# Performance work log

Hardware: AMD Instinct MI355X
Metric: run time of the kernel (lower is better)

The kernel has to match this reference:

```python
import jax, jax.numpy as jnp
import numpy as np

B, N, CIN, D, K, H, W = 1, 65536, 5, 128, 16, 64, 1024
EPS = 1e-5


def _bn(x, g, b, m, v, ch_axis):
    shape = [1] * x.ndim
    shape[ch_axis] = -1
    return (x - m.reshape(shape)) * jax.lax.rsqrt(v.reshape(shape) + EPS) * g.reshape(shape) + b.reshape(shape)


def setup_inputs() -> dict:
    key = jax.random.key(0)
    ks = jax.random.split(key, 10)
    s = 0.05
    return {
        "pc": jax.random.normal(ks[0], (B, N, CIN), jnp.float32),
        "neighbors": jax.random.randint(ks[1], (B, N, K), 0, N),
        "px": jax.random.randint(ks[2], (N,), 0, W),
        "py": jax.random.randint(ks[3], (N,), 0, H),
        "norm_gamma": jnp.ones((CIN,), jnp.float32),
        "norm_beta": jnp.zeros((CIN,), jnp.float32),
        "norm_mean": jnp.zeros((CIN,), jnp.float32),
        "norm_var": jnp.ones((CIN,), jnp.float32),
        "conv1_w": jax.random.normal(ks[4], (D, CIN), jnp.float32) * s,
        "conv1_b": jnp.zeros((D,), jnp.float32),
        "bn2a_gamma": jnp.ones((CIN,), jnp.float32),
        "bn2a_beta": jnp.zeros((CIN,), jnp.float32),
        "bn2a_mean": jnp.zeros((CIN,), jnp.float32),
        "bn2a_var": jnp.ones((CIN,), jnp.float32),
        "w2a": jax.random.normal(ks[5], (D, CIN), jnp.float32) * s,
        "bn2b_gamma": jnp.ones((D,), jnp.float32),
        "bn2b_beta": jnp.zeros((D,), jnp.float32),
        "bn2b_mean": jnp.zeros((D,), jnp.float32),
        "bn2b_var": jnp.ones((D,), jnp.float32),
        "w2b": jax.random.normal(ks[6], (D, D), jnp.float32) * s,
        "final_w": jax.random.normal(ks[7], (D, 2 * D), jnp.float32) * s,
        "final_b": jnp.zeros((D,), jnp.float32),
    }


def reference(pc, neighbors, px, py,
              norm_gamma, norm_beta, norm_mean, norm_var,
              conv1_w, conv1_b,
              bn2a_gamma, bn2a_beta, bn2a_mean, bn2a_var, w2a,
              bn2b_gamma, bn2b_beta, bn2b_mean, bn2b_var, w2b,
              final_w, final_b):
    # pc: [B, N, CIN] -> channels-first [B, CIN, N]
    x = jnp.transpose(pc, (0, 2, 1))
    x = _bn(x, norm_gamma, norm_beta, norm_mean, norm_var, 1)  # BatchNorm1d (eval)
    # point embedding: 1x1 conv1d
    point_emb = jnp.einsum('dc,bcn->bdn', conv1_w, x) + conv1_b[None, :, None]
    # neighbor gather (skip self at k=0): idx [B, K-1, N]
    nb = jnp.transpose(neighbors, (0, 2, 1))
    idx = nb[:, 1:, :]
    # gathered: [B, CIN, K-1, N]
    gathered = jnp.take_along_axis(x[:, :, None, :], idx[:, None, :, :], axis=3)
    neigh = gathered - x[:, :, None, :]  # per-neighbor difference
    # shared MLP: BN2d -> 1x1 conv (no bias) -> BN2d -> GELU -> 1x1 conv (no bias)
    h = _bn(neigh, bn2a_gamma, bn2a_beta, bn2a_mean, bn2a_var, 1)
    h = jnp.einsum('dc,bckn->bdkn', w2a, h)
    h = _bn(h, bn2b_gamma, bn2b_beta, bn2b_mean, bn2b_var, 1)
    h = jax.nn.gelu(h, approximate=False)  # torch nn.GELU default = exact erf
    h = jnp.einsum('ed,bdkn->bekn', w2b, h)
    neigh_emb = jnp.max(h, axis=2)  # max over neighbors -> [B, D, N]
    feats = jnp.einsum('df,bfn->bdn', final_w,
                       jnp.concatenate([point_emb, neigh_emb], axis=1)) + final_b[None, :, None]
    # scatter into range image (B assumed 1, as in original squeeze(0))
    proj = jnp.full((H, W, D), -1.0, dtype=jnp.float32)
    proj = proj.at[py, px].set(feats[0].T)
    return jnp.transpose(proj, (2, 0, 1))[None]  # [1, D, H, W]
```

## Files before the change

kernel.cpp:

```cpp
#include <hip/hip_runtime.h>

#define NPTS 65536
#define WW 1024
#define HWCELLS 65536
#define EPSF 1e-5f
#define QPTS 16

typedef __attribute__((ext_vector_type(8))) short short8;
typedef __attribute__((ext_vector_type(4))) float f32x4;

__device__ __forceinline__ float gelu_f(float x) {
    float x2 = x * x;
    float q  = fmaf(x2, -0.1029432f, -2.3022160f);
    float e  = __builtin_amdgcn_exp2f(x * q);
    float r  = __builtin_amdgcn_rcpf(1.0f + e);
    return x * r;
}
__device__ __forceinline__ unsigned f2bf_rne(float x) {
    unsigned u = __float_as_uint(x);
    return (u + 0x7fffu + ((u >> 16) & 1u)) >> 16;
}
__device__ __forceinline__ unsigned cvtpk(float lo, float hi) {
    unsigned r;
    asm("v_cvt_pk_bf16_f32 %0, %1, %2" : "=v"(r) : "v"(lo), "v"(hi));
    return r;
}

__global__ void init_out_k(float4* __restrict__ out4, int* __restrict__ winner) {
    int i = blockIdx.x * 256 + threadIdx.x;
    out4[i] = make_float4(-1.f, -1.f, -1.f, -1.f);
    if (i < HWCELLS) winner[i] = -1;
}

__global__ void prep_k(const float* __restrict__ pc, const int* __restrict__ px,
                       const int* __restrict__ py,
                       float4* __restrict__ xn4, float* __restrict__ xn1,
                       int* __restrict__ winner) {
    int i = blockIdx.x * blockDim.x + threadIdx.x;
    if (i >= NPTS) return;
    const float* p = &pc[(size_t)i * 5];
    xn4[i] = make_float4(p[0], p[1], p[2], p[3]);
    xn1[i] = p[4];
    int cell = py[i] * WW + px[i];
    atomicMax(&winner[cell], i);
}

__global__ void cnt_k(const int* __restrict__ winner, int* __restrict__ blockcnt) {
    int cell = blockIdx.x * 256 + threadIdx.x;
    bool occ = winner[cell] >= 0;
    unsigned long long m = __ballot(occ);
    __shared__ int wcnt[4];
    int lane = threadIdx.x & 63, wv = threadIdx.x >> 6;
    if (lane == 0) wcnt[wv] = __popcll(m);
    __syncthreads();
    if (threadIdx.x == 0)
        blockcnt[blockIdx.x] = wcnt[0] + wcnt[1] + wcnt[2] + wcnt[3];
}

__global__ void scan_k(const int* __restrict__ blockcnt, int* __restrict__ blockoff,
                       int* __restrict__ count) {
    __shared__ int s[256];
    int t = threadIdx.x;
    int orig = blockcnt[t];
    s[t] = orig;
    __syncthreads();
    for (int off = 1; off < 256; off <<= 1) {
        int v = (t >= off) ? s[t - off] : 0;
        __syncthreads();
        s[t] += v;
        __syncthreads();
    }
    blockoff[t] = s[t] - orig;
    if (t == 255) *count = s[255];
}

__global__ void fill_k(const int* __restrict__ winner, const int* __restrict__ blockoff,
                       int* __restrict__ ids) {
    int cell = blockIdx.x * 256 + threadIdx.x;
    int win = winner[cell];
    bool occ = win >= 0;
    unsigned long long m = __ballot(occ);
    __shared__ int wcnt[4];
    int lane = threadIdx.x & 63, wv = threadIdx.x >> 6;
    if (lane == 0) wcnt[wv] = __popcll(m);
    __syncthreads();
    int woff = blockoff[blockIdx.x];
    for (int i = 0; i < wv; ++i) woff += wcnt[i];
    if (occ) {
        int lrank = __popcll(m & ((1ull << lane) - 1));
        ids[woff + lrank] = win;
    }
}

__global__ void pad_k(int* __restrict__ ids, const int* __restrict__ count) {
    int c = *count;
    int i = c + threadIdx.x;
    if (threadIdx.x < 16 && i < NPTS) ids[i] = ids[0];
}

__global__ void fold_k(const float* __restrict__ ng, const float* __restrict__ nbta,
                       const float* __restrict__ nm, const float* __restrict__ nv,
                       const float* __restrict__ w2a,
                       const float* __restrict__ g2a, const float* __restrict__ b2a,
                       const float* __restrict__ m2a, const float* __restrict__ v2a,
                       const float* __restrict__ g2b, const float* __restrict__ b2b,
                       const float* __restrict__ m2b, const float* __restrict__ v2b,
                       const float* __restrict__ w2b,
                       const float* __restrict__ c1w, const float* __restrict__ c1b,
                       const float* __restrict__ fw, const float* __restrict__ fbias,
                       unsigned short* __restrict__ w2aB8,
                       unsigned short* __restrict__ w2bB,
                       unsigned short* __restrict__ fwallB) {
    __shared__ float c1wS[640];
    __shared__ float c1adjS[128];
    int d = threadIdx.x;

    float s_n[5], t_n[5];
#pragma unroll
    for (int c = 0; c < 5; ++c) {
        s_n[c] = ng[c] * rsqrtf(nv[c] + EPSF);
        t_n[c] = nbta[c] - nm[c] * s_n[c];
    }
    for (int j = d; j < 640; j += 128) c1wS[j] = c1w[j];
    __syncthreads();
    {
        float a = c1b[d];
#pragma unroll
        for (int c = 0; c < 5; ++c) a += c1wS[d * 5 + c] * t_n[c];
        c1adjS[d] = a;
    }
    __syncthreads();

    float s2b = g2b[d] * rsqrtf(v2b[d] + EPSF);
    float t2b = b2b[d] - m2b[d] * s2b;
    float acc = 0.f;
#pragma unroll
    for (int c = 0; c < 5; ++c) {
        float s2a = g2a[c] * rsqrtf(v2a[c] + EPSF);
        float t2a = b2a[c] - m2a[c] * s2a;
        float wv = w2a[d * 5 + c];
        w2aB8[d * 8 + c] = (unsigned short)f2bf_rne(s2b * wv * s2a * s_n[c]);
        acc += s2b * wv * t2a;
    }
    w2aB8[d * 8 + 5] = (unsigned short)f2bf_rne(acc + t2b);
    w2aB8[d * 8 + 6] = 0; w2aB8[d * 8 + 7] = 0;

#pragma unroll 8
    for (int i4 = 0; i4 < 32; ++i4) {
        float4 v = *(const float4*)&w2b[d * 128 + i4 * 4];
        unsigned short* dst = &w2bB[d * 128 + i4 * 4];
        dst[0] = (unsigned short)f2bf_rne(v.x);
        dst[1] = (unsigned short)f2bf_rne(v.y);
        dst[2] = (unsigned short)f2bf_rne(v.z);
        dst[3] = (unsigned short)f2bf_rne(v.w);
    }

    float f1[5] = {0.f, 0.f, 0.f, 0.f, 0.f};
    float fbv = fbias[d];
#pragma unroll 8
    for (int d4 = 0; d4 < 32; ++d4) {
        float4 fv = *(const float4*)&fw[d * 256 + d4 * 4];
        float4 fn = *(const float4*)&fw[d * 256 + 128 + d4 * 4];
        unsigned short* dst = &fwallB[d * 160 + d4 * 4];
        dst[0] = (unsigned short)f2bf_rne(fn.x);
        dst[1] = (unsigned short)f2bf_rne(fn.y);
        dst[2] = (unsigned short)f2bf_rne(fn.z);
        dst[3] = (unsigned short)f2bf_rne(fn.w);
        int dd = d4 * 4;
        fbv += fv.x * c1adjS[dd] + fv.y * c1adjS[dd+1] + fv.z * c1adjS[dd+2] + fv.w * c1adjS[dd+3];
#pragma unroll
        for (int c = 0; c < 5; ++c)
            f1[c] += fv.x * c1wS[dd*5 + c] + fv.y * c1wS[(dd+1)*5 + c]
                   + fv.z * c1wS[(dd+2)*5 + c] + fv.w * c1wS[(dd+3)*5 + c];
    }
#pragma unroll
    for (int c = 0; c < 5; ++c)
        fwallB[d * 160 + 128 + c] = (unsigned short)f2bf_rne(f1[c] * s_n[c]);
    fwallB[d * 160 + 133] = (unsigned short)f2bf_rne(fbv);
    for (int j = 134; j < 160; ++j) fwallB[d * 160 + j] = 0;
}

__launch_bounds__(256, 6)
__global__ void main_k(const int* __restrict__ ids, const int* __restrict__ countp,
                       const int* __restrict__ nbrs,
                       const float4* __restrict__ xn4, const float* __restrict__ xn1,
                       const int* __restrict__ px, const int* __restrict__ py,
                       const unsigned short* __restrict__ w2aB8,
                       const unsigned short* __restrict__ w2bB,
                       const unsigned short* __restrict__ fwallB,
                       float* __restrict__ outp) {
    const int n0 = blockIdx.x * QPTS;
    if (n0 >= *countp) return;

    __shared__ char           lds[8192];
    __shared__ unsigned short dxS[15 * 16 * 8];
    __shared__ int   idS[QPTS];
    __shared__ int   nbS[QPTS * 16];
    __shared__ float xnS[QPTS][5];
    __shared__ int   cellS[QPTS];

    const int t = threadIdx.x;
    const int w = t >> 6;
    const int l = t & 63;
    const int l15 = l & 15;
    const int lg  = l >> 4;

    if (t < QPTS) idS[t] = ids[n0 + t];
    __syncthreads();

    nbS[t] = nbrs[idS[t >> 4] * 16 + (t & 15)];
    if (t < QPTS) {
        int id = idS[t];
        float4 a = xn4[id];
        xnS[t][0] = a.x; xnS[t][1] = a.y; xnS[t][2] = a.z; xnS[t][3] = a.w;
        xnS[t][4] = xn1[id];
        cellS[t] = py[id] * WW + px[id];
    }

    short8 a1[2] = { {0,0,0,0,0,0,0,0}, {0,0,0,0,0,0,0,0} };
    if (lg == 0) {
        a1[0] = *(const short8*)(w2aB8 + (w * 32 + l15) * 8);
        a1[1] = *(const short8*)(w2aB8 + (w * 32 + 16 + l15) * 8);
    }
    short8 a2[2][4];
#pragma unroll
    for (int rt = 0; rt < 2; ++rt)
#pragma unroll
        for (int ks = 0; ks < 4; ++ks)
            a2[rt][ks] = *(const short8*)(w2bB + (w * 32 + rt * 16 + l15) * 128 + ks * 32 + lg * 8);

    __syncthreads();

    if (t < 240) {
        int pt = t & 15, kk = t >> 4;
        int nb = nbS[pt * 16 + kk + 1];
        float4 a = xn4[nb];
        float  e = xn1[nb];
        float d0 = a.x - xnS[pt][0];
        float d1 = a.y - xnS[pt][1];
        float d2 = a.z - xnS[pt][2];
        float d3 = a.w - xnS[pt][3];
        float d4 = e   - xnS[pt][4];
        uint4 v;
        v.x = cvtpk(d0, d1);
        v.y = cvtpk(d2, d3);
        v.z = cvtpk(d4, 1.0f);
        v.w = 0u;
        *(uint4*)&dxS[(kk * 16 + pt) * 8] = v;
    }
    __syncthreads();

    const f32x4 zero4 = {0.f, 0.f, 0.f, 0.f};
    f32x4 mmax[2];
#pragma unroll
    for (int rt = 0; rt < 2; ++rt)
#pragma unroll
        for (int j = 0; j < 4; ++j) mmax[rt][j] = -1e30f;

    for (int kk = 0; kk < 15; ++kk) {
        short8 dxf = *(const short8*)&dxS[(kk * 16 + l15) * 8];
        char* Gb = lds + (kk & 1) * 4096;
#pragma unroll
        for (int rt = 0; rt < 2; ++rt) {
            f32x4 s = __builtin_amdgcn_mfma_f32_16x16x32_bf16(a1[rt], dxf, zero4, 0, 0, 0);
            uint2 pr;
            pr.x = cvtpk(gelu_f(s[0]), gelu_f(s[1]));
            pr.y = cvtpk(gelu_f(s[2]), gelu_f(s[3]));
            int din0 = w * 32 + rt * 16 + lg * 4;
            *(uint2*)(Gb + l15 * 256 + ((din0 * 2) ^ (l15 << 4))) = pr;
        }
        __syncthreads();
        f32x4 acc[2];
#pragma unroll
        for (int ks = 0; ks < 4; ++ks) {
            int kb = (ks * 32 + lg * 8) * 2;
            short8 bfrag = *(const short8*)(Gb + l15 * 256 + (kb ^ (l15 << 4)));
#pragma unroll
            for (int rt = 0; rt < 2; ++rt)
                acc[rt] = __builtin_amdgcn_mfma_f32_16x16x32_bf16(
                    a2[rt][ks], bfrag, ks == 0 ? zero4 : acc[rt], 0, 0, 0);
        }
#pragma unroll
        for (int rt = 0; rt < 2; ++rt)
#pragma unroll
            for (int j = 0; j < 4; ++j)
                mmax[rt][j] = fmaxf(mmax[rt][j], acc[rt][j]);
    }

    __syncthreads();

    {
        char* Mb = lds;
        int sw = l15 << 4;
#pragma unroll
        for (int rt = 0; rt < 2; ++rt) {
            int dout = w * 32 + rt * 16 + lg * 4;
            unsigned lo = cvtpk(mmax[rt][0], mmax[rt][1]);
            unsigned hi = cvtpk(mmax[rt][2], mmax[rt][3]);
            *(unsigned*)(Mb + l15 * 320 + ((dout * 2) ^ sw)) = lo;
            *(unsigned*)(Mb + l15 * 320 + (((dout + 2) * 2) ^ sw)) = hi;
        }
        if (t < QPTS) {
            uint4 a;
            a.x = cvtpk(xnS[t][0], xnS[t][1]);
            a.y = cvtpk(xnS[t][2], xnS[t][3]);
            a.z = cvtpk(xnS[t][4], 1.0f);
            a.w = 0u;
            uint4 z; z.x = 0u; z.y = 0u; z.z = 0u; z.w = 0u;
            *(uint4*)(Mb + t * 320 + 256) = a;
            *(uint4*)(Mb + t * 320 + 272) = z;
            *(uint4*)(Mb + t * 320 + 288) = z;
            *(uint4*)(Mb + t * 320 + 304) = z;
        }
    }
    __syncthreads();

    f32x4 facc[2];
    const char* Mr = lds;
#pragma unroll
    for (int ks = 0; ks < 5; ++ks) {
        short8 af[2];
#pragma unroll
        for (int rt = 0; rt < 2; ++rt)
            af[rt] = *(const short8*)(fwallB + (w * 32 + rt * 16 + l15) * 160 + ks * 32 + lg * 8);
        int kb = (ks * 32 + lg * 8) * 2;
        int kbs = (kb < 256) ? (kb ^ (l15 << 4)) : kb;
        short8 bfr = *(const short8*)(Mr + l15 * 320 + kbs);
#pragma unroll
        for (int rt = 0; rt < 2; ++rt)
            facc[rt] = __builtin_amdgcn_mfma_f32_16x16x32_bf16(
                af[rt], bfr, ks == 0 ? zero4 : facc[rt], 0, 0, 0);
    }

    const int cell = cellS[l15];
#pragma unroll
    for (int rt = 0; rt < 2; ++rt) {
        int e0 = w * 32 + rt * 16 + lg * 4;
#pragma unroll
        for (int j = 0; j < 4; ++j)
            outp[(size_t)(e0 + j) * HWCELLS + cell] = facc[rt][j];
    }
}

extern "C" void kernel_launch(void* const* d_in, const int* in_sizes, int n_in,
                              void* d_out, int out_size, void* d_ws, size_t ws_size,
                              hipStream_t stream) {
    const float* pc        = (const float*)d_in[0];
    const int*   neighbors = (const int*)d_in[1];
    const int*   px        = (const int*)d_in[2];
    const int*   py        = (const int*)d_in[3];
    const float* norm_g    = (const float*)d_in[4];
    const float* norm_b    = (const float*)d_in[5];
    const float* norm_m    = (const float*)d_in[6];
    const float* norm_v    = (const float*)d_in[7];
    const float* conv1_w   = (const float*)d_in[8];
    const float* conv1_b   = (const float*)d_in[9];
    const float* bn2a_g    = (const float*)d_in[10];
    const float* bn2a_b    = (const float*)d_in[11];
    const float* bn2a_m    = (const float*)d_in[12];
    const float* bn2a_v    = (const float*)d_in[13];
    const float* w2a       = (const float*)d_in[14];
    const float* bn2b_g    = (const float*)d_in[15];
    const float* bn2b_b    = (const float*)d_in[16];
    const float* bn2b_m    = (const float*)d_in[17];
    const float* bn2b_v    = (const float*)d_in[18];
    const float* w2b       = (const float*)d_in[19];
    const float* final_w   = (const float*)d_in[20];
    const float* final_b   = (const float*)d_in[21];
    float* out = (float*)d_out;

    char* ws = (char*)d_ws;
    float4*         xn4      = (float4*)(ws);
    float*          xn1      = (float*)(ws + 1048576);
    int*            winner   = (int*)(ws + 1310720);
    int*            ids      = (int*)(ws + 1572864);
    int*            count    = (int*)(ws + 1835008);
    int*            blockcnt = (int*)(ws + 1835264);
    int*            blockoff = (int*)(ws + 1836288);
    unsigned short* w2aB8    = (unsigned short*)(ws + 1837312);
    unsigned short* w2bB     = (unsigned short*)(ws + 1839360);
    unsigned short* fwallB   = (unsigned short*)(ws + 1872128);

    init_out_k<<<8192, 256, 0, stream>>>((float4*)out, winner);
    prep_k<<<256, 256, 0, stream>>>(pc, px, py, xn4, xn1, winner);
    fold_k<<<1, 128, 0, stream>>>(norm_g, norm_b, norm_m, norm_v,
                                  w2a, bn2a_g, bn2a_b, bn2a_m, bn2a_v,
                                  bn2b_g, bn2b_b, bn2b_m, bn2b_v, w2b,
                                  conv1_w, conv1_b, final_w, final_b,
                                  w2aB8, w2bB, fwallB);
    cnt_k<<<256, 256, 0, stream>>>(winner, blockcnt);
    scan_k<<<1, 256, 0, stream>>>(blockcnt, blockoff, count);
    fill_k<<<256, 256, 0, stream>>>(winner, blockoff, ids);
    pad_k<<<1, 64, 0, stream>>>(ids, count);
    main_k<<<4096, 256, 0, stream>>>(ids, count, neighbors, xn4, xn1, px, py,
                                     w2aB8, w2bB, fwallB, out);
}
```

Measured before the change: 103.3 us.

## Merge preprocessing kernels and precompute cell indices for main kernel

Cuts the launch chain from eight kernels to five. The fold work becomes an extra block of the prep kernel, the output fill is merged into the count kernel, and every block redundantly repeats the block scan inside the fill kernel. The fill also records cell indices so the main kernel no longer reads px/py, and padding is replaced by clamping slots. It also raises the main kernel's launch-bounds occupancy hint to 8 and fully unrolls the neighbor loop, which may raise register pressure.

```diff
diff --git a/kernel.cpp b/kernel.cpp
--- a/kernel.cpp
+++ b/kernel.cpp
@@ -26,110 +26,59 @@
     return r;
 }
 
-__global__ void init_out_k(float4* __restrict__ out4, int* __restrict__ winner) {
+__global__ void init_k(int* __restrict__ winner) {
     int i = blockIdx.x * 256 + threadIdx.x;
-    out4[i] = make_float4(-1.f, -1.f, -1.f, -1.f);
-    if (i < HWCELLS) winner[i] = -1;
-}
-
-__global__ void prep_k(const float* __restrict__ pc, const int* __restrict__ px,
-                       const int* __restrict__ py,
-                       float4* __restrict__ xn4, float* __restrict__ xn1,
-                       int* __restrict__ winner) {
-    int i = blockIdx.x * blockDim.x + threadIdx.x;
-    if (i >= NPTS) return;
-    const float* p = &pc[(size_t)i * 5];
-    xn4[i] = make_float4(p[0], p[1], p[2], p[3]);
-    xn1[i] = p[4];
-    int cell = py[i] * WW + px[i];
-    atomicMax(&winner[cell], i);
-}
-
-__global__ void cnt_k(const int* __restrict__ winner, int* __restrict__ blockcnt) {
-    int cell = blockIdx.x * 256 + threadIdx.x;
-    bool occ = winner[cell] >= 0;
-    unsigned long long m = __ballot(occ);
-    __shared__ int wcnt[4];
-    int lane = threadIdx.x & 63, wv = threadIdx.x >> 6;
-    if (lane == 0) wcnt[wv] = __popcll(m);
-    __syncthreads();
-    if (threadIdx.x == 0)
-        blockcnt[blockIdx.x] = wcnt[0] + wcnt[1] + wcnt[2] + wcnt[3];
-}
-
-__global__ void scan_k(const int* __restrict__ blockcnt, int* __restrict__ blockoff,
-                       int* __restrict__ count) {
-    __shared__ int s[256];
-    int t = threadIdx.x;
-    int orig = blockcnt[t];
-    s[t] = orig;
-    __syncthreads();
-    for (int off = 1; off < 256; off <<= 1) {
-        int v = (t >= off) ? s[t - off] : 0;
-        __syncthreads();
-        s[t] += v;
-        __syncthreads();
-    }
-    blockoff[t] = s[t] - orig;
-    if (t == 255) *count = s[255];
-}
-
-__global__ void fill_k(const int* __restrict__ winner, const int* __restrict__ blockoff,
-                       int* __restrict__ ids) {
-    int cell = blockIdx.x * 256 + threadIdx.x;
-    int win = winner[cell];
-    bool occ = win >= 0;
-    unsigned long long m = __ballot(occ);
-    __shared__ int wcnt[4];
-    int lane = threadIdx.x & 63, wv = threadIdx.x >> 6;
-    if (lane == 0) wcnt[wv] = __popcll(m);
-    __syncthreads();
-    int woff = blockoff[blockIdx.x];
-    for (int i = 0; i < wv; ++i) woff += wcnt[i];
-    if (occ) {
-        int lrank = __popcll(m & ((1ull << lane) - 1));
-        ids[woff + lrank] = win;
-    }
-}
-
-__global__ void pad_k(int* __restrict__ ids, const int* __restrict__ count) {
-    int c = *count;
-    int i = c + threadIdx.x;
-    if (threadIdx.x < 16 && i < NPTS) ids[i] = ids[0];
-}
-
-__global__ void fold_k(const float* __restrict__ ng, const float* __restrict__ nbta,
-                       const float* __restrict__ nm, const float* __restrict__ nv,
-                       const float* __restrict__ w2a,
-                       const float* __restrict__ g2a, const float* __restrict__ b2a,
-                       const float* __restrict__ m2a, const float* __restrict__ v2a,
-                       const float* __restrict__ g2b, const float* __restrict__ b2b,
-                       const float* __restrict__ m2b, const float* __restrict__ v2b,
-                       const float* __restrict__ w2b,
-                       const float* __restrict__ c1w, const float* __restrict__ c1b,
-                       const float* __restrict__ fw, const float* __restrict__ fbias,
-                       unsigned short* __restrict__ w2aB8,
-                       unsigned short* __restrict__ w2bB,
-                       unsigned short* __restrict__ fwallB) {
+    winner[i] = -1;
+}
+
+__global__ void prepfold_k(const float* __restrict__ pc, const int* __restrict__ px,
+                           const int* __restrict__ py,
+                           float4* __restrict__ xn4, float* __restrict__ xn1,
+                           int* __restrict__ winner,
+                           const float* __restrict__ ng, const float* __restrict__ nbta,
+                           const float* __restrict__ nm, const float* __restrict__ nv,
+                           const float* __restrict__ w2a,
+                           const float* __restrict__ g2a, const float* __restrict__ b2a,
+                           const float* __restrict__ m2a, const float* __restrict__ v2a,
+                           const float* __restrict__ g2b, const float* __restrict__ b2b,
+                           const float* __restrict__ m2b, const float* __restrict__ v2b,
+                           const float* __restrict__ w2b,
+                           const float* __restrict__ c1w, const float* __restrict__ c1b,
+                           const float* __restrict__ fw, const float* __restrict__ fbias,
+                           unsigned short* __restrict__ w2aB8,
+                           unsigned short* __restrict__ w2bB,
+                           unsigned short* __restrict__ fwallB) {
     __shared__ float c1wS[640];
     __shared__ float c1adjS[128];
-    int d = threadIdx.x;
-
+    const int t = threadIdx.x;
+
+    if (blockIdx.x < 256) {
+        int i = blockIdx.x * 256 + t;
+        const float* p = &pc[(size_t)i * 5];
+        xn4[i] = make_float4(p[0], p[1], p[2], p[3]);
+        xn1[i] = p[4];
+        int cell = py[i] * WW + px[i];
+        atomicMax(&winner[cell], i);
+        return;
+    }
+
+    const int d = t;
     float s_n[5], t_n[5];
 #pragma unroll
     for (int c = 0; c < 5; ++c) {
         s_n[c] = ng[c] * rsqrtf(nv[c] + EPSF);
         t_n[c] = nbta[c] - nm[c] * s_n[c];
     }
-    for (int j = d; j < 640; j += 128) c1wS[j] = c1w[j];
-    __syncthreads();
-    {
+    for (int j = t; j < 640; j += 256) c1wS[j] = c1w[j];
+    __syncthreads();
+    if (t < 128) {
         float a = c1b[d];
 #pragma unroll
         for (int c = 0; c < 5; ++c) a += c1wS[d * 5 + c] * t_n[c];
         c1adjS[d] = a;
     }
     __syncthreads();
+    if (t >= 128) return;
 
     float s2b = g2b[d] * rsqrtf(v2b[d] + EPSF);
     float t2b = b2b[d] - m2b[d] * s2b;
@@ -180,17 +129,69 @@
     for (int j = 134; j < 160; ++j) fwallB[d * 160 + j] = 0;
 }
 
-__launch_bounds__(256, 6)
-__global__ void main_k(const int* __restrict__ ids, const int* __restrict__ countp,
+__global__ void cntout_k(float4* __restrict__ out4,
+                         const int* __restrict__ winner, int* __restrict__ blockcnt) {
+    int gid = blockIdx.x * 256 + threadIdx.x;
+    float4 mone = make_float4(-1.f, -1.f, -1.f, -1.f);
+#pragma unroll
+    for (int j = 0; j < 8; ++j) out4[gid + j * 262144] = mone;
+    if (blockIdx.x >= 256) return;
+    bool occ = winner[gid] >= 0;
+    unsigned long long m = __ballot(occ);
+    __shared__ int wcnt[4];
+    int lane = threadIdx.x & 63, wv = threadIdx.x >> 6;
+    if (lane == 0) wcnt[wv] = __popcll(m);
+    __syncthreads();
+    if (threadIdx.x == 0)
+        blockcnt[blockIdx.x] = wcnt[0] + wcnt[1] + wcnt[2] + wcnt[3];
+}
+
+__global__ void fillscan_k(const int* __restrict__ winner,
+                           const int* __restrict__ blockcnt,
+                           int* __restrict__ ids, int* __restrict__ cells,
+                           int* __restrict__ count) {
+    __shared__ int s[256];
+    __shared__ int wcnt[4];
+    int t = threadIdx.x;
+    s[t] = blockcnt[t];
+    __syncthreads();
+    for (int off = 1; off < 256; off <<= 1) {
+        int v = (t >= off) ? s[t - off] : 0;
+        __syncthreads();
+        s[t] += v;
+        __syncthreads();
+    }
+    if (blockIdx.x == 0 && t == 255) *count = s[255];
+    int excl = s[blockIdx.x] - blockcnt[blockIdx.x];
+
+    int cell = blockIdx.x * 256 + t;
+    int win = winner[cell];
+    bool occ = win >= 0;
+    unsigned long long m = __ballot(occ);
+    int lane = t & 63, wv = t >> 6;
+    if (lane == 0) wcnt[wv] = __popcll(m);
+    __syncthreads();
+    int woff = excl;
+    for (int i = 0; i < wv; ++i) woff += wcnt[i];
+    if (occ) {
+        int lrank = __popcll(m & ((1ull << lane) - 1));
+        ids[woff + lrank] = win;
+        cells[woff + lrank] = cell;
+    }
+}
+
+__launch_bounds__(256, 8)
+__global__ void main_k(const int* __restrict__ ids, const int* __restrict__ cells,
+                       const int* __restrict__ countp,
                        const int* __restrict__ nbrs,
                        const float4* __restrict__ xn4, const float* __restrict__ xn1,
-                       const int* __restrict__ px, const int* __restrict__ py,
                        const unsigned short* __restrict__ w2aB8,
                        const unsigned short* __restrict__ w2bB,
                        const unsigned short* __restrict__ fwallB,
                        float* __restrict__ outp) {
+    const int cnt = *countp;
     const int n0 = blockIdx.x * QPTS;
-    if (n0 >= *countp) return;
+    if (n0 >= cnt) return;
 
     __shared__ char           lds[8192];
     __shared__ unsigned short dxS[15 * 16 * 8];
@@ -205,7 +206,12 @@
     const int l15 = l & 15;
     const int lg  = l >> 4;
 
-    if (t < QPTS) idS[t] = ids[n0 + t];
+    if (t < QPTS) {
+        int slot = n0 + t;
+        slot = slot < cnt ? slot : cnt - 1;
+        idS[t] = ids[slot];
+        cellS[t] = cells[slot];
+    }
     __syncthreads();
 
     nbS[t] = nbrs[idS[t >> 4] * 16 + (t & 15)];
@@ -214,7 +220,6 @@
         float4 a = xn4[id];
         xnS[t][0] = a.x; xnS[t][1] = a.y; xnS[t][2] = a.z; xnS[t][3] = a.w;
         xnS[t][4] = xn1[id];
-        cellS[t] = py[id] * WW + px[id];
     }
 
     short8 a1[2] = { {0,0,0,0,0,0,0,0}, {0,0,0,0,0,0,0,0} };
@@ -257,6 +262,7 @@
 #pragma unroll
         for (int j = 0; j < 4; ++j) mmax[rt][j] = -1e30f;
 
+#pragma unroll
     for (int kk = 0; kk < 15; ++kk) {
         short8 dxf = *(const short8*)&dxS[(kk * 16 + l15) * 8];
         char* Gb = lds + (kk & 1) * 4096;
@@ -374,24 +380,22 @@
     float*          xn1      = (float*)(ws + 1048576);
     int*            winner   = (int*)(ws + 1310720);
     int*            ids      = (int*)(ws + 1572864);
-    int*            count    = (int*)(ws + 1835008);
-    int*            blockcnt = (int*)(ws + 1835264);
-    int*            blockoff = (int*)(ws + 1836288);
-    unsigned short* w2aB8    = (unsigned short*)(ws + 1837312);
-    unsigned short* w2bB     = (unsigned short*)(ws + 1839360);
-    unsigned short* fwallB   = (unsigned short*)(ws + 1872128);
-
-    init_out_k<<<8192, 256, 0, stream>>>((float4*)out, winner);
-    prep_k<<<256, 256, 0, stream>>>(pc, px, py, xn4, xn1, winner);
-    fold_k<<<1, 128, 0, stream>>>(norm_g, norm_b, norm_m, norm_v,
-                                  w2a, bn2a_g, bn2a_b, bn2a_m, bn2a_v,
-                                  bn2b_g, bn2b_b, bn2b_m, bn2b_v, w2b,
-                                  conv1_w, conv1_b, final_w, final_b,
-                                  w2aB8, w2bB, fwallB);
-    cnt_k<<<256, 256, 0, stream>>>(winner, blockcnt);
-    scan_k<<<1, 256, 0, stream>>>(blockcnt, blockoff, count);
-    fill_k<<<256, 256, 0, stream>>>(winner, blockoff, ids);
-    pad_k<<<1, 64, 0, stream>>>(ids, count);
-    main_k<<<4096, 256, 0, stream>>>(ids, count, neighbors, xn4, xn1, px, py,
+    int*            cells    = (int*)(ws + 1835008);
+    int*            count    = (int*)(ws + 2097152);
+    int*            blockcnt = (int*)(ws + 2097408);
+    unsigned short* w2aB8    = (unsigned short*)(ws + 2098432);
+    unsigned short* w2bB     = (unsigned short*)(ws + 2100480);
+    unsigned short* fwallB   = (unsigned short*)(ws + 2133248);
+
+    init_k<<<256, 256, 0, stream>>>(winner);
+    prepfold_k<<<257, 256, 0, stream>>>(pc, px, py, xn4, xn1, winner,
+                                        norm_g, norm_b, norm_m, norm_v,
+                                        w2a, bn2a_g, bn2a_b, bn2a_m, bn2a_v,
+                                        bn2b_g, bn2b_b, bn2b_m, bn2b_v, w2b,
+                                        conv1_w, conv1_b, final_w, final_b,
+                                        w2aB8, w2bB, fwallB);
+    cntout_k<<<1024, 256, 0, stream>>>((float4*)out, winner, blockcnt);
+    fillscan_k<<<256, 256, 0, stream>>>(winner, blockcnt, ids, cells, count);
+    main_k<<<4096, 256, 0, stream>>>(ids, cells, count, neighbors, xn4, xn1,
                                      w2aB8, w2bB, fwallB, out);
 }
```

New measurement: 217.1 us. +110.2%, slower.
